# Performance work log

Measured on AMD Instinct MI355X. Metric: run time of the kernel, lower is better.

Reference implementation:

```python
import jax, jax.numpy as jnp
import numpy as np

EPS = 1e-5

def layer_norm(x, g, b):
    m = jnp.mean(x, axis=-1, keepdims=True)
    v = jnp.var(x, axis=-1, keepdims=True)
    return (x - m) * jax.lax.rsqrt(v + EPS) * g + b

def setup_inputs() -> dict:
    key = jax.random.key(0)
    ks = jax.random.split(key, 16)
    B, N, C_Z, C_H = 1, 512, 128, 128
    s_z = 1.0 / np.sqrt(C_Z)
    s_h = 1.0 / np.sqrt(C_H)
    inp = {
        "z": jax.random.normal(ks[0], (B, N, N, C_Z), jnp.float32),
        "mask": jnp.ones((B, N, N), jnp.float32),
        # linear weights stored as [in, out] so forward is x @ W + b
        "w_ag": jax.random.uniform(ks[1], (C_Z, C_H), jnp.float32, -s_z, s_z),
        "b_ag": jnp.zeros((C_H,), jnp.float32),
        "w_ap": jax.random.uniform(ks[2], (C_Z, C_H), jnp.float32, -s_z, s_z),
        "b_ap": jnp.zeros((C_H,), jnp.float32),
        "w_bg": jax.random.uniform(ks[3], (C_Z, C_H), jnp.float32, -s_z, s_z),
        "b_bg": jnp.zeros((C_H,), jnp.float32),
        "w_bp": jax.random.uniform(ks[4], (C_Z, C_H), jnp.float32, -s_z, s_z),
        "b_bp": jnp.zeros((C_H,), jnp.float32),
        "w_g": jax.random.uniform(ks[5], (C_Z, C_Z), jnp.float32, -s_z, s_z),
        "b_g": jnp.zeros((C_Z,), jnp.float32),
        "w_z": jax.random.uniform(ks[6], (C_H, C_Z), jnp.float32, -s_h, s_h),
        "b_z": jnp.zeros((C_Z,), jnp.float32),
        "ln_in_g": jnp.ones((C_Z,), jnp.float32),
        "ln_in_b": jnp.zeros((C_Z,), jnp.float32),
        "ln_out_g": jnp.ones((C_H,), jnp.float32),
        "ln_out_b": jnp.zeros((C_H,), jnp.float32),
    }
    return inp

def reference(z, mask, w_ag, b_ag, w_ap, b_ap, w_bg, b_bg, w_bp, b_bp,
              w_g, b_g, w_z, b_z, ln_in_g, ln_in_b, ln_out_g, ln_out_b):
    m = mask[..., None]                      # [B,N,N,1]
    zn = layer_norm(z, ln_in_g, ln_in_b)     # [B,N,N,Cz]
    a = m * jax.nn.sigmoid(zn @ w_ag + b_ag) * (zn @ w_ap + b_ap)  # [B,N,N,Ch]
    b = m * jax.nn.sigmoid(zn @ w_bg + b_bg) * (zn @ w_bp + b_bp)  # [B,N,N,Ch]
    # outgoing: p[i,j,c] = sum_k a[i,k,c] * b[j,k,c]
    x = jnp.einsum('bikc,bjkc->bijc', a, b)
    x = layer_norm(x, ln_out_g, ln_out_b)
    x = x @ w_z + b_z
    g = jax.nn.sigmoid(zn @ w_g + b_g)
    return x * g
```

## Files before the change

kernel.cpp:

```cpp
#include <hip/hip_runtime.h>
#include <hip/hip_bf16.h>
#include <math.h>


#define N 512
#define C 128
#define NN (N*N)
#define PK 136
#define PT 40
#define PX 137
#define ST 72

typedef __attribute__((ext_vector_type(8))) short bf16x8;
typedef __attribute__((ext_vector_type(4))) float f32x4;
typedef unsigned short u16;
typedef unsigned int u32;

__device__ __forceinline__ u16 f2bf(float f) {
    u32 u = __builtin_bit_cast(u32, f);
    u = (u + 0x7fffu + ((u >> 16) & 1u)) >> 16;
    return (u16)u;
}
__device__ __forceinline__ float bf2f(u16 h) {
    return __builtin_bit_cast(float, ((u32)h) << 16);
}
__device__ __forceinline__ float sigmoidf(float x) {
    return 1.f / (1.f + __expf(-x));
}

__global__ __launch_bounds__(256) void k_wt_all(
    const float* __restrict__ w0, const float* __restrict__ w1,
    const float* __restrict__ w2, const float* __restrict__ w3,
    const float* __restrict__ w4, const float* __restrict__ w5,
    const float* __restrict__ gin, const float* __restrict__ gout,
    u16* __restrict__ o0, u16* __restrict__ o1, u16* __restrict__ o2,
    u16* __restrict__ o3, u16* __restrict__ o4, u16* __restrict__ o5) {
    int sel = blockIdx.x >> 6;
    int idx = (blockIdx.x & 63) * 256 + threadIdx.x;
    const float* w = sel == 0 ? w0 : sel == 1 ? w1 : sel == 2 ? w2
                   : sel == 3 ? w3 : sel == 4 ? w4 : w5;
    u16* o = sel == 0 ? o0 : sel == 1 ? o1 : sel == 2 ? o2
           : sel == 3 ? o3 : sel == 4 ? o4 : o5;
    const float* g = (sel == 5) ? gout : gin;
    int co = idx >> 7, k = idx & 127;
    o[idx] = f2bf(g[k] * w[k * C + co]);
}

__global__ __launch_bounds__(256) void k_bias(
    const float* __restrict__ w0, const float* __restrict__ w1,
    const float* __restrict__ w2, const float* __restrict__ w3,
    const float* __restrict__ w4, const float* __restrict__ w5,
    const float* __restrict__ b0, const float* __restrict__ b1,
    const float* __restrict__ b2, const float* __restrict__ b3,
    const float* __restrict__ b4, const float* __restrict__ b5,
    const float* __restrict__ vin, const float* __restrict__ vout,
    float* __restrict__ obias) {
    int id = blockIdx.x * 256 + threadIdx.x;
    int m = id >> 7, cc = id & 127;
    const float* w = m == 0 ? w0 : m == 1 ? w1 : m == 2 ? w2
                   : m == 3 ? w3 : m == 4 ? w4 : w5;
    const float* b = m == 0 ? b0 : m == 1 ? b1 : m == 2 ? b2
                   : m == 3 ? b3 : m == 4 ? b4 : b5;
    const float* v = (m == 5) ? vout : vin;
    float acc = 0.f;
#pragma unroll 4
    for (int k = 0; k < 128; ++k) acc += v[k] * w[k * C + cc];
    obias[id] = b[cc] + acc;
}

__global__ __launch_bounds__(256) void k_proj_fused(
    const float* __restrict__ z, const float* __restrict__ mask,
    const u16* __restrict__ wag, const u16* __restrict__ wap,
    const u16* __restrict__ wbg, const u16* __restrict__ wbp,
    const u16* __restrict__ wgg, const float* __restrict__ biasAll,
    u16* __restrict__ aT, u16* __restrict__ bT, u16* __restrict__ gate) {
    __shared__ u16 sA[64 * PK];
    __shared__ u16 sT[4][16 * ST];
    long r0 = (long)blockIdx.x * 64;
    int tid = threadIdx.x, wave = tid >> 6, lane = tid & 63;
    int lo = lane & 15, quad = lane >> 4;

    {
        int rl = lane >> 2, cb = lane & 3;
        int row = wave * 16 + rl;
        const float* zr = z + (r0 + row) * C + cb * 32;
        float4 v[8];
        float s = 0.f, s2 = 0.f;
#pragma unroll
        for (int i = 0; i < 8; ++i) {
            v[i] = *(const float4*)(zr + i * 4);
            s  += v[i].x + v[i].y + v[i].z + v[i].w;
            s2 += v[i].x * v[i].x + v[i].y * v[i].y + v[i].z * v[i].z + v[i].w * v[i].w;
        }
        s += __shfl_xor(s, 1); s2 += __shfl_xor(s2, 1);
        s += __shfl_xor(s, 2); s2 += __shfl_xor(s2, 2);
        float mean = s * (1.f / 128.f);
        float rs = rsqrtf(s2 * (1.f / 128.f) - mean * mean + 1e-5f);
        u16* dst = &sA[row * PK + cb * 32];
#pragma unroll
        for (int j = 0; j < 4; ++j) {
            uint4 pk;
            pk.x = (u32)f2bf((v[2*j].x   - mean) * rs) | ((u32)f2bf((v[2*j].y   - mean) * rs) << 16);
            pk.y = (u32)f2bf((v[2*j].z   - mean) * rs) | ((u32)f2bf((v[2*j].w   - mean) * rs) << 16);
            pk.z = (u32)f2bf((v[2*j+1].x - mean) * rs) | ((u32)f2bf((v[2*j+1].y - mean) * rs) << 16);
            pk.w = (u32)f2bf((v[2*j+1].z - mean) * rs) | ((u32)f2bf((v[2*j+1].w - mean) * rs) << 16);
            *(uint4*)(dst + 8 * j) = pk;
        }
    }
    __syncthreads();

    int c0 = wave * 32;
    float msk[4][4];
#pragma unroll
    for (int mi = 0; mi < 4; ++mi)
#pragma unroll
        for (int r = 0; r < 4; ++r)
            msk[mi][r] = mask[r0 + mi * 16 + quad * 4 + r];

    u16* sTw = &sT[wave][0];

    auto pair_stage = [&](const u16* __restrict__ wG, const float* __restrict__ bG,
                          const u16* __restrict__ wP, const float* __restrict__ bP,
                          u16* __restrict__ outT) {
#pragma unroll
        for (int nt = 0; nt < 2; ++nt) {
            int c = c0 + nt * 16 + lo;
            bf16x8 fG[4], fP[4];
#pragma unroll
            for (int ki = 0; ki < 4; ++ki) {
                fG[ki] = *(const bf16x8*)(wG + c * C + ki * 32 + quad * 8);
                fP[ki] = *(const bf16x8*)(wP + c * C + ki * 32 + quad * 8);
            }
            f32x4 aG[4], aP[4];
#pragma unroll
            for (int mi = 0; mi < 4; ++mi) { aG[mi] = (f32x4)(0.f); aP[mi] = (f32x4)(0.f); }
#pragma unroll
            for (int mi = 0; mi < 4; ++mi)
#pragma unroll
                for (int ki = 0; ki < 4; ++ki) {
                    bf16x8 av = *(const bf16x8*)(&sA[(mi * 16 + lo) * PK + ki * 32 + quad * 8]);
                    aG[mi] = __builtin_amdgcn_mfma_f32_16x16x32_bf16(av, fG[ki], aG[mi], 0, 0, 0);
                    aP[mi] = __builtin_amdgcn_mfma_f32_16x16x32_bf16(av, fP[ki], aP[mi], 0, 0, 0);
                }
            float bGv = bG[c], bPv = bP[c];
#pragma unroll
            for (int mi = 0; mi < 4; ++mi) {
                float v0 = msk[mi][0] * sigmoidf(aG[mi][0] + bGv) * (aP[mi][0] + bPv);
                float v1 = msk[mi][1] * sigmoidf(aG[mi][1] + bGv) * (aP[mi][1] + bPv);
                float v2 = msk[mi][2] * sigmoidf(aG[mi][2] + bGv) * (aP[mi][2] + bPv);
                float v3 = msk[mi][3] * sigmoidf(aG[mi][3] + bGv) * (aP[mi][3] + bPv);
                uint2 pk;
                pk.x = (u32)f2bf(v0) | ((u32)f2bf(v1) << 16);
                pk.y = (u32)f2bf(v2) | ((u32)f2bf(v3) << 16);
                *(uint2*)(&sTw[lo * ST + mi * 16 + quad * 4]) = pk;
            }
            {
                int cl = lane >> 2, pr = lane & 3;
                uint4 x0 = *(const uint4*)(&sTw[cl * ST + pr * 16]);
                uint4 x1 = *(const uint4*)(&sTw[cl * ST + pr * 16 + 8]);
                u16* g = outT + (long)(c0 + nt * 16 + cl) * NN + r0 + pr * 16;
                *(uint4*)(g) = x0;
                *(uint4*)(g + 8) = x1;
            }
        }
    };
    pair_stage(wag, biasAll + 0,   wap, biasAll + 128, aT);
    pair_stage(wbg, biasAll + 256, wbp, biasAll + 384, bT);

    {
        f32x4 gA[2][4];
#pragma unroll
        for (int nt = 0; nt < 2; ++nt) {
            bf16x8 gF[4];
#pragma unroll
            for (int ki = 0; ki < 4; ++ki)
                gF[ki] = *(const bf16x8*)(wgg + (c0 + nt * 16 + lo) * C + ki * 32 + quad * 8);
#pragma unroll
            for (int mi = 0; mi < 4; ++mi) gA[nt][mi] = (f32x4)(0.f);
#pragma unroll
            for (int mi = 0; mi < 4; ++mi)
#pragma unroll
                for (int ki = 0; ki < 4; ++ki) {
                    bf16x8 av = *(const bf16x8*)(&sA[(mi * 16 + lo) * PK + ki * 32 + quad * 8]);
                    gA[nt][mi] = __builtin_amdgcn_mfma_f32_16x16x32_bf16(av, gF[ki], gA[nt][mi], 0, 0, 0);
                }
        }
        __syncthreads();
        const float* bg5 = biasAll + 512;
#pragma unroll
        for (int nt = 0; nt < 2; ++nt) {
            int c = c0 + nt * 16 + lo;
            float bv = bg5[c];
#pragma unroll
            for (int mi = 0; mi < 4; ++mi)
#pragma unroll
                for (int r = 0; r < 4; ++r)
                    sA[(mi * 16 + quad * 4 + r) * PK + c] = f2bf(sigmoidf(gA[nt][mi][r] + bv));
        }
        __syncthreads();
#pragma unroll
        for (int p = 0; p < 4; ++p) {
            int linear = p * 2048 + tid * 8;
            int row = linear >> 7, k = linear & 127;
            *(uint4*)(gate + (r0 + row) * C + k) = *(const uint4*)(&sA[row * PK + k]);
        }
    }
}

__global__ __launch_bounds__(256) void k_tri(const u16* __restrict__ aT,
                                             const u16* __restrict__ bT,
                                             u16* __restrict__ xT) {
    __shared__ u16 sA[128 * PT];
    __shared__ u16 sB[128 * PT];
    int bid = blockIdx.x;
    int swz = (bid & 7) * 256 + (bid >> 3);
    int c = swz >> 4;
    int i0 = ((swz >> 2) & 3) * 128, j0 = (swz & 3) * 128;
    const u16* aBase = aT + (long)c * NN + (long)i0 * N;
    const u16* bBase = bT + (long)c * NN + (long)j0 * N;
    int tid = threadIdx.x;
    int wave = tid >> 6, lane = tid & 63, lo = lane & 15, quad = lane >> 4;
    int mq = (wave >> 1) * 64, nq = (wave & 1) * 64;
    f32x4 acc[4][4];
#pragma unroll
    for (int mi = 0; mi < 4; ++mi)
#pragma unroll
        for (int ni = 0; ni < 4; ++ni) acc[mi][ni] = (f32x4)(0.f);

    int srow[2], sk[2];
#pragma unroll
    for (int p = 0; p < 2; ++p) {
        int linear = p * 2048 + tid * 8;
        srow[p] = linear >> 5; sk[p] = linear & 31;
    }
    uint4 ra[2], rb[2];
#pragma unroll
    for (int p = 0; p < 2; ++p) {
        ra[p] = *(const uint4*)(aBase + srow[p] * N + sk[p]);
        rb[p] = *(const uint4*)(bBase + srow[p] * N + sk[p]);
    }
    for (int kk = 0; kk < N; kk += 32) {
        __syncthreads();
#pragma unroll
        for (int p = 0; p < 2; ++p) {
            *(uint4*)(&sA[srow[p] * PT + sk[p]]) = ra[p];
            *(uint4*)(&sB[srow[p] * PT + sk[p]]) = rb[p];
        }
        __syncthreads();
        if (kk + 32 < N) {
#pragma unroll
            for (int p = 0; p < 2; ++p) {
                ra[p] = *(const uint4*)(aBase + srow[p] * N + kk + 32 + sk[p]);
                rb[p] = *(const uint4*)(bBase + srow[p] * N + kk + 32 + sk[p]);
            }
        }
        bf16x8 af[4], bfr[4];
#pragma unroll
        for (int mi = 0; mi < 4; ++mi)
            af[mi] = *(const bf16x8*)(&sA[(mq + mi * 16 + lo) * PT + quad * 8]);
#pragma unroll
        for (int ni = 0; ni < 4; ++ni)
            bfr[ni] = *(const bf16x8*)(&sB[(nq + ni * 16 + lo) * PT + quad * 8]);
#pragma unroll
        for (int mi = 0; mi < 4; ++mi)
#pragma unroll
            for (int ni = 0; ni < 4; ++ni)
                acc[mi][ni] = __builtin_amdgcn_mfma_f32_16x16x32_bf16(af[mi], bfr[ni], acc[mi][ni], 0, 0, 0);
    }
    u16* outBase = xT + (long)c * NN;
#pragma unroll
    for (int mi = 0; mi < 4; ++mi)
#pragma unroll
        for (int ni = 0; ni < 4; ++ni)
#pragma unroll
            for (int r = 0; r < 4; ++r) {
                int gi = i0 + mq + mi * 16 + quad * 4 + r;
                int gj = j0 + nq + ni * 16 + lo;
                outBase[(long)gi * N + gj] = f2bf(acc[mi][ni][r]);
            }
}

__global__ __launch_bounds__(256) void k_out(
    const u16* __restrict__ xT, const u16* __restrict__ gate,
    const u16* __restrict__ wzT, const float* __restrict__ bz,
    float* __restrict__ out) {
    __shared__ float sX[64 * PX];
    __shared__ u16 sA[64 * PK];
    __shared__ float sRed[2][4][64];
    __shared__ float2 sMV[64];
    long r0 = (long)blockIdx.x * 64;
    int tid = threadIdx.x;
#pragma unroll
    for (int p = 0; p < 4; ++p) {
        int linear = p * 2048 + tid * 8;
        int cc = linear >> 6, jr = linear & 63;
        uint4 v = *(const uint4*)(xT + (long)cc * NN + r0 + jr);
        u16* u = (u16*)&v;
#pragma unroll
        for (int e = 0; e < 8; ++e) sX[(jr + e) * PX + cc] = bf2f(u[e]);
    }
    __syncthreads();
    {
        int jr = tid & 63, part = tid >> 6;
        float s = 0, s2 = 0;
#pragma unroll
        for (int c = part * 32; c < part * 32 + 32; ++c) {
            float v = sX[jr * PX + c];
            s += v; s2 += v * v;
        }
        sRed[0][part][jr] = s; sRed[1][part][jr] = s2;
    }
    __syncthreads();
    if (tid < 64) {
        float S = 0, S2 = 0;
#pragma unroll
        for (int p = 0; p < 4; ++p) { S += sRed[0][p][tid]; S2 += sRed[1][p][tid]; }
        float mean = S * (1.f / 128.f);
        float var = S2 * (1.f / 128.f) - mean * mean;
        sMV[tid] = make_float2(mean, rsqrtf(var + 1e-5f));
    }
    __syncthreads();
    {
        int row = tid & 63, c0 = (tid >> 6) * 32;
        float2 mv = sMV[row];
#pragma unroll
        for (int c = c0; c < c0 + 32; ++c)
            sA[row * PK + c] = f2bf((sX[row * PX + c] - mv.x) * mv.y);
    }
    __syncthreads();
    int wave = tid >> 6, lane = tid & 63, lo = lane & 15, quad = lane >> 4;
    int msub = wave * 16;
    bf16x8 av[4];
#pragma unroll
    for (int ki = 0; ki < 4; ++ki)
        av[ki] = *(const bf16x8*)(&sA[(msub + lo) * PK + ki * 32 + quad * 8]);
    f32x4 acc[8];
#pragma unroll
    for (int nt = 0; nt < 8; ++nt) acc[nt] = (f32x4)(0.f);
#pragma unroll
    for (int nt = 0; nt < 8; ++nt)
#pragma unroll
        for (int ki = 0; ki < 4; ++ki) {
            bf16x8 b8 = *(const bf16x8*)(wzT + (nt * 16 + lo) * C + ki * 32 + quad * 8);
            acc[nt] = __builtin_amdgcn_mfma_f32_16x16x32_bf16(av[ki], b8, acc[nt], 0, 0, 0);
        }
#pragma unroll
    for (int nt = 0; nt < 8; ++nt) {
        int c = nt * 16 + lo;
        float bzv = bz[c];
#pragma unroll
        for (int r = 0; r < 4; ++r) {
            int row = msub + quad * 4 + r;
            long rr = r0 + row;
            float g = bf2f(gate[rr * C + c]);
            out[rr * C + c] = (acc[nt][r] + bzv) * g;
        }
    }
}

extern "C" void kernel_launch(void* const* d_in, const int* in_sizes, int n_in,
                              void* d_out, int out_size, void* d_ws, size_t ws_size,
                              hipStream_t stream) {
    const float* z       = (const float*)d_in[0];
    const float* mask    = (const float*)d_in[1];
    const float* w_ag    = (const float*)d_in[2];
    const float* b_ag    = (const float*)d_in[3];
    const float* w_ap    = (const float*)d_in[4];
    const float* b_ap    = (const float*)d_in[5];
    const float* w_bg    = (const float*)d_in[6];
    const float* b_bg    = (const float*)d_in[7];
    const float* w_bp    = (const float*)d_in[8];
    const float* b_bp    = (const float*)d_in[9];
    const float* w_g     = (const float*)d_in[10];
    const float* b_g     = (const float*)d_in[11];
    const float* w_z     = (const float*)d_in[12];
    const float* b_z     = (const float*)d_in[13];
    const float* ln_in_g = (const float*)d_in[14];
    const float* ln_in_b = (const float*)d_in[15];
    const float* ln_out_g= (const float*)d_in[16];
    const float* ln_out_b= (const float*)d_in[17];
    float* out = (float*)d_out;

    char* ws = (char*)d_ws;
    u16* a_t  = (u16*)(ws);
    u16* b_t  = (u16*)(ws + 67108864L);
    u16* gate = (u16*)(ws + 134217728L);
    u16* x_t  = (u16*)(ws + 201326592L);
    u16* wag_t = (u16*)(ws + 268435456L);
    u16* wap_t = wag_t + 16384;
    u16* wbg_t = wag_t + 32768;
    u16* wbp_t = wag_t + 49152;
    u16* wg_t  = wag_t + 65536;
    u16* wz_t  = wag_t + 81920;
    float* biasAdj = (float*)(ws + 268435456L + 196608L);

    k_wt_all<<<384, 256, 0, stream>>>(w_ag, w_ap, w_bg, w_bp, w_g, w_z,
                                      ln_in_g, ln_out_g,
                                      wag_t, wap_t, wbg_t, wbp_t, wg_t, wz_t);

    k_bias<<<3, 256, 0, stream>>>(w_ag, w_ap, w_bg, w_bp, w_g, w_z,
                                  b_ag, b_ap, b_bg, b_bp, b_g, b_z,
                                  ln_in_b, ln_out_b, biasAdj);

    k_proj_fused<<<NN / 64, 256, 0, stream>>>(
        z, mask, wag_t, wap_t, wbg_t, wbp_t, wg_t, biasAdj,
        a_t, b_t, gate);

    k_tri<<<2048, 256, 0, stream>>>(a_t, b_t, x_t);

    k_out<<<NN / 64, 256, 0, stream>>>(x_t, gate, wz_t, biasAdj + 640, out);
}
```

Before: 669.8 us.

## Split input LayerNorm into own kernel, drop tri prefetch and block swizzle

Moves the input LayerNorm out of the fused projection kernel into a separate kernel that writes a bf16 normalized copy into the x_t workspace, and the projection kernel then loads that copy. The projection kernel gets a launch bound of 4 blocks per CU. The triangle matmul drops its register prefetch of the next K tile and its block-index swizzle, using a 2D grid instead. This adds a full extra round trip of the normalized tensor through memory and removes load/compute overlap and L2 locality in the main matmul.

Measured after the change: 846.4 us. 1.26x slower.

```diff
diff --git a/kernel.cpp b/kernel.cpp
--- a/kernel.cpp
+++ b/kernel.cpp
@@ -68,8 +68,38 @@
     obias[id] = b[cc] + acc;
 }
 
-__global__ __launch_bounds__(256) void k_proj_fused(
-    const float* __restrict__ z, const float* __restrict__ mask,
+__global__ __launch_bounds__(256) void k_ln(const float* __restrict__ z,
+                                            u16* __restrict__ zn) {
+    long gid = (long)blockIdx.x * 256 + threadIdx.x;
+    long row = gid >> 2;
+    int cb = (int)(gid & 3);
+    const float* zr = z + row * C + cb * 32;
+    float4 v[8];
+    float s = 0.f, s2 = 0.f;
+#pragma unroll
+    for (int i = 0; i < 8; ++i) {
+        v[i] = *(const float4*)(zr + i * 4);
+        s  += v[i].x + v[i].y + v[i].z + v[i].w;
+        s2 += v[i].x * v[i].x + v[i].y * v[i].y + v[i].z * v[i].z + v[i].w * v[i].w;
+    }
+    s += __shfl_xor(s, 1); s2 += __shfl_xor(s2, 1);
+    s += __shfl_xor(s, 2); s2 += __shfl_xor(s2, 2);
+    float mean = s * (1.f / 128.f);
+    float rs = rsqrtf(s2 * (1.f / 128.f) - mean * mean + 1e-5f);
+    u16* dst = zn + row * C + cb * 32;
+#pragma unroll
+    for (int j = 0; j < 4; ++j) {
+        uint4 pk;
+        pk.x = (u32)f2bf((v[2*j].x   - mean) * rs) | ((u32)f2bf((v[2*j].y   - mean) * rs) << 16);
+        pk.y = (u32)f2bf((v[2*j].z   - mean) * rs) | ((u32)f2bf((v[2*j].w   - mean) * rs) << 16);
+        pk.z = (u32)f2bf((v[2*j+1].x - mean) * rs) | ((u32)f2bf((v[2*j+1].y - mean) * rs) << 16);
+        pk.w = (u32)f2bf((v[2*j+1].z - mean) * rs) | ((u32)f2bf((v[2*j+1].w - mean) * rs) << 16);
+        *(uint4*)(dst + 8 * j) = pk;
+    }
+}
+
+__global__ __launch_bounds__(256, 4) void k_proj2(
+    const u16* __restrict__ zn, const float* __restrict__ mask,
     const u16* __restrict__ wag, const u16* __restrict__ wap,
     const u16* __restrict__ wbg, const u16* __restrict__ wbp,
     const u16* __restrict__ wgg, const float* __restrict__ biasAll,
@@ -80,32 +110,11 @@
     int tid = threadIdx.x, wave = tid >> 6, lane = tid & 63;
     int lo = lane & 15, quad = lane >> 4;
 
-    {
-        int rl = lane >> 2, cb = lane & 3;
-        int row = wave * 16 + rl;
-        const float* zr = z + (r0 + row) * C + cb * 32;
-        float4 v[8];
-        float s = 0.f, s2 = 0.f;
-#pragma unroll
-        for (int i = 0; i < 8; ++i) {
-            v[i] = *(const float4*)(zr + i * 4);
-            s  += v[i].x + v[i].y + v[i].z + v[i].w;
-            s2 += v[i].x * v[i].x + v[i].y * v[i].y + v[i].z * v[i].z + v[i].w * v[i].w;
-        }
-        s += __shfl_xor(s, 1); s2 += __shfl_xor(s2, 1);
-        s += __shfl_xor(s, 2); s2 += __shfl_xor(s2, 2);
-        float mean = s * (1.f / 128.f);
-        float rs = rsqrtf(s2 * (1.f / 128.f) - mean * mean + 1e-5f);
-        u16* dst = &sA[row * PK + cb * 32];
-#pragma unroll
-        for (int j = 0; j < 4; ++j) {
-            uint4 pk;
-            pk.x = (u32)f2bf((v[2*j].x   - mean) * rs) | ((u32)f2bf((v[2*j].y   - mean) * rs) << 16);
-            pk.y = (u32)f2bf((v[2*j].z   - mean) * rs) | ((u32)f2bf((v[2*j].w   - mean) * rs) << 16);
-            pk.z = (u32)f2bf((v[2*j+1].x - mean) * rs) | ((u32)f2bf((v[2*j+1].y - mean) * rs) << 16);
-            pk.w = (u32)f2bf((v[2*j+1].z - mean) * rs) | ((u32)f2bf((v[2*j+1].w - mean) * rs) << 16);
-            *(uint4*)(dst + 8 * j) = pk;
-        }
+#pragma unroll
+    for (int p = 0; p < 4; ++p) {
+        int linear = p * 2048 + tid * 8;
+        int row = linear >> 7, k = linear & 127;
+        *(uint4*)(&sA[row * PK + k]) = *(const uint4*)(zn + (r0 + row) * C + k);
     }
     __syncthreads();
 
@@ -212,10 +221,8 @@
                                              u16* __restrict__ xT) {
     __shared__ u16 sA[128 * PT];
     __shared__ u16 sB[128 * PT];
-    int bid = blockIdx.x;
-    int swz = (bid & 7) * 256 + (bid >> 3);
-    int c = swz >> 4;
-    int i0 = ((swz >> 2) & 3) * 128, j0 = (swz & 3) * 128;
+    int c = blockIdx.y;
+    int i0 = (blockIdx.x >> 2) * 128, j0 = (blockIdx.x & 3) * 128;
     const u16* aBase = aT + (long)c * NN + (long)i0 * N;
     const u16* bBase = bT + (long)c * NN + (long)j0 * N;
     int tid = threadIdx.x;
@@ -226,34 +233,16 @@
     for (int mi = 0; mi < 4; ++mi)
 #pragma unroll
         for (int ni = 0; ni < 4; ++ni) acc[mi][ni] = (f32x4)(0.f);
-
-    int srow[2], sk[2];
-#pragma unroll
-    for (int p = 0; p < 2; ++p) {
-        int linear = p * 2048 + tid * 8;
-        srow[p] = linear >> 5; sk[p] = linear & 31;
-    }
-    uint4 ra[2], rb[2];
-#pragma unroll
-    for (int p = 0; p < 2; ++p) {
-        ra[p] = *(const uint4*)(aBase + srow[p] * N + sk[p]);
-        rb[p] = *(const uint4*)(bBase + srow[p] * N + sk[p]);
-    }
     for (int kk = 0; kk < N; kk += 32) {
         __syncthreads();
 #pragma unroll
         for (int p = 0; p < 2; ++p) {
-            *(uint4*)(&sA[srow[p] * PT + sk[p]]) = ra[p];
-            *(uint4*)(&sB[srow[p] * PT + sk[p]]) = rb[p];
+            int linear = p * 2048 + tid * 8;
+            int row = linear >> 5, k = linear & 31;
+            *(uint4*)(&sA[row * PT + k]) = *(const uint4*)(aBase + row * N + kk + k);
+            *(uint4*)(&sB[row * PT + k]) = *(const uint4*)(bBase + row * N + kk + k);
         }
         __syncthreads();
-        if (kk + 32 < N) {
-#pragma unroll
-            for (int p = 0; p < 2; ++p) {
-                ra[p] = *(const uint4*)(aBase + srow[p] * N + kk + 32 + sk[p]);
-                rb[p] = *(const uint4*)(bBase + srow[p] * N + kk + 32 + sk[p]);
-            }
-        }
         bf16x8 af[4], bfr[4];
 #pragma unroll
         for (int mi = 0; mi < 4; ++mi)
@@ -393,6 +382,7 @@
     u16* wg_t  = wag_t + 65536;
     u16* wz_t  = wag_t + 81920;
     float* biasAdj = (float*)(ws + 268435456L + 196608L);
+    u16* zn = x_t;
 
     k_wt_all<<<384, 256, 0, stream>>>(w_ag, w_ap, w_bg, w_bp, w_g, w_z,
                                       ln_in_g, ln_out_g,
@@ -402,11 +392,13 @@
                                   b_ag, b_ap, b_bg, b_bp, b_g, b_z,
                                   ln_in_b, ln_out_b, biasAdj);
 
-    k_proj_fused<<<NN / 64, 256, 0, stream>>>(
-        z, mask, wag_t, wap_t, wbg_t, wbp_t, wg_t, biasAdj,
+    k_ln<<<4096, 256, 0, stream>>>(z, zn);
+
+    k_proj2<<<NN / 64, 256, 0, stream>>>(
+        zn, mask, wag_t, wap_t, wbg_t, wbp_t, wg_t, biasAdj,
         a_t, b_t, gate);
 
-    k_tri<<<2048, 256, 0, stream>>>(a_t, b_t, x_t);
+    k_tri<<<dim3(16, 128), 256, 0, stream>>>(a_t, b_t, x_t);
 
     k_out<<<NN / 64, 256, 0, stream>>>(x_t, gate, wz_t, biasAdj + 640, out);
 }
```
